# Optimization experiments

Hardware: AMD Instinct MI355X
Metric: run time of the kernel (lower is better)

## Reference

```python
import jax, jax.numpy as jnp
import numpy as np
import math

SIZE = (60, 270, 480)           # full video T, H, W
CHANNELS = 14                   # sum of per-level grid channels 8+4+2
GRID_SIZES = [(60, 16, 16, 8), (30, 8, 8, 4), (15, 4, 4, 2)]
IDX_MAX = (60, 3, 5)            # patch grid -> patch_size (1, 90, 96)
PADDING = (0, 1, 1)
N_PATCH = 64
MANIP_LBASE = 2.0
MANIP_LEVELS = 8
INIT_SCALE = 1e-3


def setup_inputs() -> dict:
    key = jax.random.key(0)
    kt, kh, kw = jax.random.split(key, 3)
    idx = jnp.stack([
        jax.random.randint(kt, (N_PATCH,), 0, IDX_MAX[0]),
        jax.random.randint(kh, (N_PATCH,), 0, IDX_MAX[1]),
        jax.random.randint(kw, (N_PATCH,), 0, IDX_MAX[2]),
    ], axis=1).astype(jnp.int32)
    inp = {
        "idx": idx,
        "idx_max": jnp.asarray(IDX_MAX, dtype=jnp.int32),
        "padding": jnp.asarray(PADDING, dtype=jnp.int32),
    }
    for i, (T, H, W, C) in enumerate(GRID_SIZES):
        k = jax.random.fold_in(key, 10 + i)
        inp[f"grid{i}"] = jax.random.normal(k, (T * H * W, C), jnp.float32) * INIT_SCALE
    return inp


def _pixel_idx_1d(ix, size_d, nmax_d, pad_d):
    # ix: [N] patch index along one dim -> ([N, P+2*pad] clipped pixel idx, mask)
    p = size_d // nmax_d
    offs = jnp.arange(-pad_d, p + pad_d)
    raw = ix[:, None] * p + offs[None, :]
    mask = ((raw >= 0) & (raw < size_d)).astype(jnp.float32)
    return jnp.clip(raw, 0, size_d - 1), mask


def reference(idx, idx_max, padding, grid0, grid1, grid2):
    T, H, W = SIZE
    im = tuple(int(v) for v in np.asarray(idx_max))
    pad = tuple(int(v) for v in np.asarray(padding))
    patch = tuple(SIZE[d] // im[d] for d in range(3))
    ppad = tuple(patch[d] + 2 * pad[d] for d in range(3))

    # Multi-level grids -> trilinear upsample to full (T,H,W,C_i), concat on C.
    # jax.image.resize 'trilinear' uses half-pixel centers == torch align_corners=False.
    enc_splits = []
    for g, (Tg, Hg, Wg, Cg) in zip((grid0, grid1, grid2), GRID_SIZES):
        enc_splits.append(jax.image.resize(g.reshape(Tg, Hg, Wg, Cg), (T, H, W, Cg), method="trilinear"))
    enc = jnp.concatenate(enc_splits, axis=-1).reshape(T * H * W, CHANNELS)

    it, mt = _pixel_idx_1d(idx[:, 0], T, im[0], pad[0])
    ih, mh = _pixel_idx_1d(idx[:, 1], H, im[1], pad[1])
    iw, mw = _pixel_idx_1d(idx[:, 2], W, im[2], pad[2])

    flat = (it[:, :, None, None] * (H * W) + ih[:, None, :, None] * W + iw[:, None, None, :]).reshape(-1)
    mask = (mt[:, :, None, None] * mh[:, None, :, None] * mw[:, None, None, :]).reshape(-1, 1)

    t_embed = (mask * enc[flat]).reshape((idx.shape[0],) + ppad + (CHANNELS,))

    bases = (MANIP_LBASE ** jnp.arange(MANIP_LEVELS, dtype=jnp.float32)) * math.pi
    v = idx[:, 0].astype(jnp.float32)[:, None] * bases
    t_manip = jnp.concatenate([jnp.sin(v), jnp.cos(v)], axis=-1)  # [N, 2*levels]

    return t_embed, t_manip
```

## Files before the change

### kernel.cpp

```cpp
#include <hip/hip_runtime.h>
#include <math.h>


#define N_PATCH 64
#define PPAD_H 92
#define PPAD_W 98
#define CH 14
#define PIX_PER_PATCH (PPAD_H * PPAD_W)
#define ROWS_PER_BLOCK 2
#define BLOCKS_PER_PATCH 46
#define PX_PER_BLOCK 196
#define F4_PER_BLOCK (PX_PER_BLOCK * CH / 4)
#define ELEMS_PER_PATCH (PIX_PER_PATCH * CH)
#define ELEMS_PER_BLOCK (PX_PER_BLOCK * CH)
#define TOTAL_EMBED (N_PATCH * ELEMS_PER_PATCH)
#define TOTAL_MANIP (N_PATCH * 16)

#define RB_STRIDE 72
#define L1_OFF 48
#define L2_OFF 64

__device__ __forceinline__ float lerpf(float a, float b, float f) {
    return a + f * (b - a);
}

__device__ __forceinline__ int wcell0(int rw0, float sw, int Wg) {
    float x = ((float)rw0 + 0.5f) * sw - 0.5f;
    int w0 = (int)floorf(x);
    return min(max(w0, 0), Wg - 1);
}

__global__ __launch_bounds__(256) void embed_kernel(
    const int* __restrict__ idx,
    const float* __restrict__ g0,
    const float* __restrict__ g1,
    const float* __restrict__ g2,
    float* __restrict__ out)
{
    __shared__ __align__(16) float s_V[ROWS_PER_BLOCK * RB_STRIDE];
    __shared__ __align__(16) float s_buf[PX_PER_BLOCK * CH];

    const int tid = threadIdx.x;
    const int bx  = blockIdx.x;
    const int n   = blockIdx.y;
    const int it  = idx[3 * n + 0];
    const int ih  = idx[3 * n + 1];
    const int iw  = idx[3 * n + 2];
    const int rw0 = iw * 96 - 1;

    const float sw0 = (float)((double)16 / 480.0);
    const float sw1 = (float)((double)8  / 480.0);
    const float sw2 = (float)((double)4  / 480.0);
    const float sh0 = (float)((double)16 / 270.0);
    const float sh1 = (float)((double)8  / 270.0);
    const float sh2 = (float)((double)4  / 270.0);

    const int C0_0 = wcell0(rw0, sw0, 16);
    const int C0_1 = wcell0(rw0, sw1, 8);
    const int C0_2 = wcell0(rw0, sw2, 4);

    if (bx == 0 && n == 0) {
        float* om = out + TOTAL_EMBED;
        for (int e = tid; e < TOTAL_MANIP; e += 256) {
            int nn = e >> 4;
            int j  = e & 15;
            int l  = j & 7;
            float base = (float)M_PI * (float)(1 << l);
            float v = (float)idx[3 * nn + 0] * base;
            double dv = (double)v;
            om[e] = (float)((j < 8) ? sin(dv) : cos(dv));
        }
    }

    if (tid < 96) {
        int chn  = tid & 7;
        int u    = tid >> 3;
        int row  = (u >= 6);
        int cell = u - 6 * row;
        int rh   = ih * 90 + (bx * 2 + row) - 1;
        float mh = ((unsigned)rh < 270u) ? 1.0f : 0.0f;
        float xh = ((float)rh + 0.5f) * sh0 - 0.5f;
        float ff = floorf(xh);
        float fh = xh - ff;
        int h0 = (int)ff;
        int h0c = min(max(h0, 0), 15), h1c = min(h0 + 1, 15);
        int cw = min(C0_0 + cell, 15);
        const float* base = g0 + (size_t)it * 2048;
        float a = base[(h0c * 16 + cw) * 8 + chn];
        float b = base[(h1c * 16 + cw) * 8 + chn];
        s_V[row * RB_STRIDE + cell * 8 + chn] = mh * lerpf(a, b, fh);
    } else if (tid < 128) {
        int i    = tid - 96;
        int chn  = i & 3;
        int u    = i >> 2;
        int row  = (u >= 4);
        int cell = u - 4 * row;
        int rh   = ih * 90 + (bx * 2 + row) - 1;
        float mh = ((unsigned)rh < 270u) ? 1.0f : 0.0f;
        float xh = ((float)rh + 0.5f) * sh1 - 0.5f;
        float ff = floorf(xh);
        float fh = xh - ff;
        int h0 = (int)ff;
        int h0c = min(max(h0, 0), 7), h1c = min(h0 + 1, 7);
        float xt = ((float)it + 0.5f) * 0.5f - 0.5f;
        float ftf = floorf(xt);
        float ft  = xt - ftf;
        int t0 = (int)ftf;
        int t0c = min(max(t0, 0), 29), t1c = min(t0 + 1, 29);
        int cw = min(C0_1 + cell, 7);
        float a00 = g1[((t0c * 8 + h0c) * 8 + cw) * 4 + chn];
        float a01 = g1[((t0c * 8 + h1c) * 8 + cw) * 4 + chn];
        float a10 = g1[((t1c * 8 + h0c) * 8 + cw) * 4 + chn];
        float a11 = g1[((t1c * 8 + h1c) * 8 + cw) * 4 + chn];
        s_V[row * RB_STRIDE + L1_OFF + cell * 4 + chn] =
            mh * lerpf(lerpf(a00, a01, fh), lerpf(a10, a11, fh), ft);
    } else if (tid < 140) {
        int i    = tid - 128;
        int chn  = i & 1;
        int u    = i >> 1;
        int row  = (u >= 3);
        int cell = u - 3 * row;
        int rh   = ih * 90 + (bx * 2 + row) - 1;
        float mh = ((unsigned)rh < 270u) ? 1.0f : 0.0f;
        float xh = ((float)rh + 0.5f) * sh2 - 0.5f;
        float ff = floorf(xh);
        float fh = xh - ff;
        int h0 = (int)ff;
        int h0c = min(max(h0, 0), 3), h1c = min(h0 + 1, 3);
        float xt = ((float)it + 0.5f) * 0.25f - 0.5f;
        float ftf = floorf(xt);
        float ft  = xt - ftf;
        int t0 = (int)ftf;
        int t0c = min(max(t0, 0), 14), t1c = min(t0 + 1, 14);
        int cw = min(C0_2 + cell, 3);
        float a00 = g2[((t0c * 4 + h0c) * 4 + cw) * 2 + chn];
        float a01 = g2[((t0c * 4 + h1c) * 4 + cw) * 2 + chn];
        float a10 = g2[((t1c * 4 + h0c) * 4 + cw) * 2 + chn];
        float a11 = g2[((t1c * 4 + h1c) * 4 + cw) * 2 + chn];
        s_V[row * RB_STRIDE + L2_OFF + cell * 2 + chn] =
            mh * lerpf(lerpf(a00, a01, fh), lerpf(a10, a11, fh), ft);
    }

    __syncthreads();

    if (tid < PX_PER_BLOCK) {
        int row = (tid >= PPAD_W);
        int ww  = tid - PPAD_W * row;
        int rw  = iw * 96 + ww - 1;
        float mw = ((unsigned)rw < 480u) ? 1.0f : 0.0f;
        float rwc = (float)rw + 0.5f;

        float x0 = rwc * sw0 - 0.5f;
        float f0f = floorf(x0);
        float fw0 = x0 - f0f;
        int w00 = (int)f0f;
        int oA0 = (min(max(w00, 0), 15) - C0_0) * 8;
        int oB0 = (min(w00 + 1, 15)    - C0_0) * 8;
        float x1 = rwc * sw1 - 0.5f;
        float f1f = floorf(x1);
        float fw1 = x1 - f1f;
        int w01 = (int)f1f;
        int oA1 = L1_OFF + (min(max(w01, 0), 7) - C0_1) * 4;
        int oB1 = L1_OFF + (min(w01 + 1, 7)     - C0_1) * 4;
        float x2 = rwc * sw2 - 0.5f;
        float f2f = floorf(x2);
        float fw2 = x2 - f2f;
        int w02 = (int)f2f;
        int oA2 = L2_OFF + (min(max(w02, 0), 3) - C0_2) * 2;
        int oB2 = L2_OFF + (min(w02 + 1, 3)     - C0_2) * 2;

        const float* V = s_V + row * RB_STRIDE;
        float4 A0  = *(const float4*)(V + oA0);
        float4 A1  = *(const float4*)(V + oA0 + 4);
        float4 B0  = *(const float4*)(V + oB0);
        float4 B1  = *(const float4*)(V + oB0 + 4);
        float4 C1a = *(const float4*)(V + oA1);
        float4 C1b = *(const float4*)(V + oB1);
        float2 C2a = *(const float2*)(V + oA2);
        float2 C2b = *(const float2*)(V + oB2);

        float2* b = (float2*)(s_buf + tid * CH);
        b[0] = make_float2(mw * lerpf(A0.x, B0.x, fw0),
                           mw * lerpf(A0.y, B0.y, fw0));
        b[1] = make_float2(mw * lerpf(A0.z, B0.z, fw0),
                           mw * lerpf(A0.w, B0.w, fw0));
        b[2] = make_float2(mw * lerpf(A1.x, B1.x, fw0),
                           mw * lerpf(A1.y, B1.y, fw0));
        b[3] = make_float2(mw * lerpf(A1.z, B1.z, fw0),
                           mw * lerpf(A1.w, B1.w, fw0));
        b[4] = make_float2(mw * lerpf(C1a.x, C1b.x, fw1),
                           mw * lerpf(C1a.y, C1b.y, fw1));
        b[5] = make_float2(mw * lerpf(C1a.z, C1b.z, fw1),
                           mw * lerpf(C1a.w, C1b.w, fw1));
        b[6] = make_float2(mw * lerpf(C2a.x, C2b.x, fw2),
                           mw * lerpf(C2a.y, C2b.y, fw2));
    }
    __syncthreads();

    const float4* sb = (const float4*)s_buf;
    float4* gb = (float4*)(out + (size_t)n * ELEMS_PER_PATCH + bx * ELEMS_PER_BLOCK);
    for (int j = tid; j < F4_PER_BLOCK; j += 256) gb[j] = sb[j];
}

extern "C" void kernel_launch(void* const* d_in, const int* in_sizes, int n_in,
                              void* d_out, int out_size, void* d_ws, size_t ws_size,
                              hipStream_t stream) {
    const int*   idx = (const int*)  d_in[0];
    const float* g0  = (const float*)d_in[3];
    const float* g1  = (const float*)d_in[4];
    const float* g2  = (const float*)d_in[5];
    float* out = (float*)d_out;

    dim3 grid(BLOCKS_PER_PATCH, N_PATCH);
    embed_kernel<<<grid, 256, 0, stream>>>(idx, g0, g1, g2, out);
}
```

Before: 12.64 us.

## Process two patches per block, overlapping one tile's store with next compute

Each block now handles two patches (n and n+32), halving the grid. The row-interpolation stage for both patches is done in one loop, then the first tile is computed, stored while the second tile is computed, and the second tile is stored. This aims to amortize per-block setup and overlap global stores with compute, at the cost of fewer blocks (1472 vs 2944), double shared memory, and more serialized work per block.

Result: slower. 14.07 us (+11.3%).

```diff
diff --git a/kernel.cpp b/kernel.cpp
--- a/kernel.cpp
+++ b/kernel.cpp
@@ -3,6 +3,7 @@
 
 
 #define N_PATCH 64
+#define HALF_N 32
 #define PPAD_H 92
 #define PPAD_W 98
 #define CH 14
@@ -37,16 +38,15 @@
     const float* __restrict__ g2,
     float* __restrict__ out)
 {
-    __shared__ __align__(16) float s_V[ROWS_PER_BLOCK * RB_STRIDE];
-    __shared__ __align__(16) float s_buf[PX_PER_BLOCK * CH];
+    __shared__ __align__(16) float s_V0[ROWS_PER_BLOCK * RB_STRIDE];
+    __shared__ __align__(16) float s_V1[ROWS_PER_BLOCK * RB_STRIDE];
+    __shared__ __align__(16) float s_buf0[PX_PER_BLOCK * CH];
+    __shared__ __align__(16) float s_buf1[PX_PER_BLOCK * CH];
 
     const int tid = threadIdx.x;
     const int bx  = blockIdx.x;
-    const int n   = blockIdx.y;
-    const int it  = idx[3 * n + 0];
-    const int ih  = idx[3 * n + 1];
-    const int iw  = idx[3 * n + 2];
-    const int rw0 = iw * 96 - 1;
+    const int n0  = blockIdx.y;
+    const int n1  = blockIdx.y + HALF_N;
 
     const float sw0 = (float)((double)16 / 480.0);
     const float sw1 = (float)((double)8  / 480.0);
@@ -55,11 +55,14 @@
     const float sh1 = (float)((double)8  / 270.0);
     const float sh2 = (float)((double)4  / 270.0);
 
-    const int C0_0 = wcell0(rw0, sw0, 16);
-    const int C0_1 = wcell0(rw0, sw1, 8);
-    const int C0_2 = wcell0(rw0, sw2, 4);
-
-    if (bx == 0 && n == 0) {
+    const int it0 = idx[3 * n0 + 0], ih0 = idx[3 * n0 + 1], iw0 = idx[3 * n0 + 2];
+    const int it1 = idx[3 * n1 + 0], ih1 = idx[3 * n1 + 1], iw1 = idx[3 * n1 + 2];
+    const int rw0a = iw0 * 96 - 1;
+    const int rw0b = iw1 * 96 - 1;
+    const int C00a = wcell0(rw0a, sw0, 16), C01a = wcell0(rw0a, sw1, 8), C02a = wcell0(rw0a, sw2, 4);
+    const int C00b = wcell0(rw0b, sw0, 16), C01b = wcell0(rw0b, sw1, 8), C02b = wcell0(rw0b, sw2, 4);
+
+    if (bx == 0 && blockIdx.y == 0) {
         float* om = out + TOTAL_EMBED;
         for (int e = tid; e < TOTAL_MANIP; e += 256) {
             int nn = e >> 4;
@@ -72,81 +75,80 @@
         }
     }
 
-    if (tid < 96) {
-        int chn  = tid & 7;
-        int u    = tid >> 3;
-        int row  = (u >= 6);
-        int cell = u - 6 * row;
-        int rh   = ih * 90 + (bx * 2 + row) - 1;
+    for (int e = tid; e < 280; e += 256) {
+        int t   = (e >= 140);
+        int oa  = e - 140 * t;
+        int row = (oa >= 70);
+        int off = oa - 70 * row;
+        int itq = t ? it1 : it0;
+        int ihq = t ? ih1 : ih0;
+        float* sV = t ? s_V1 : s_V0;
+        int rh  = ihq * 90 + (bx * 2 + row) - 1;
         float mh = ((unsigned)rh < 270u) ? 1.0f : 0.0f;
-        float xh = ((float)rh + 0.5f) * sh0 - 0.5f;
-        float ff = floorf(xh);
-        float fh = xh - ff;
-        int h0 = (int)ff;
-        int h0c = min(max(h0, 0), 15), h1c = min(h0 + 1, 15);
-        int cw = min(C0_0 + cell, 15);
-        const float* base = g0 + (size_t)it * 2048;
-        float a = base[(h0c * 16 + cw) * 8 + chn];
-        float b = base[(h1c * 16 + cw) * 8 + chn];
-        s_V[row * RB_STRIDE + cell * 8 + chn] = mh * lerpf(a, b, fh);
-    } else if (tid < 128) {
-        int i    = tid - 96;
-        int chn  = i & 3;
-        int u    = i >> 2;
-        int row  = (u >= 4);
-        int cell = u - 4 * row;
-        int rh   = ih * 90 + (bx * 2 + row) - 1;
-        float mh = ((unsigned)rh < 270u) ? 1.0f : 0.0f;
-        float xh = ((float)rh + 0.5f) * sh1 - 0.5f;
-        float ff = floorf(xh);
-        float fh = xh - ff;
-        int h0 = (int)ff;
-        int h0c = min(max(h0, 0), 7), h1c = min(h0 + 1, 7);
-        float xt = ((float)it + 0.5f) * 0.5f - 0.5f;
-        float ftf = floorf(xt);
-        float ft  = xt - ftf;
-        int t0 = (int)ftf;
-        int t0c = min(max(t0, 0), 29), t1c = min(t0 + 1, 29);
-        int cw = min(C0_1 + cell, 7);
-        float a00 = g1[((t0c * 8 + h0c) * 8 + cw) * 4 + chn];
-        float a01 = g1[((t0c * 8 + h1c) * 8 + cw) * 4 + chn];
-        float a10 = g1[((t1c * 8 + h0c) * 8 + cw) * 4 + chn];
-        float a11 = g1[((t1c * 8 + h1c) * 8 + cw) * 4 + chn];
-        s_V[row * RB_STRIDE + L1_OFF + cell * 4 + chn] =
-            mh * lerpf(lerpf(a00, a01, fh), lerpf(a10, a11, fh), ft);
-    } else if (tid < 140) {
-        int i    = tid - 128;
-        int chn  = i & 1;
-        int u    = i >> 1;
-        int row  = (u >= 3);
-        int cell = u - 3 * row;
-        int rh   = ih * 90 + (bx * 2 + row) - 1;
-        float mh = ((unsigned)rh < 270u) ? 1.0f : 0.0f;
-        float xh = ((float)rh + 0.5f) * sh2 - 0.5f;
-        float ff = floorf(xh);
-        float fh = xh - ff;
-        int h0 = (int)ff;
-        int h0c = min(max(h0, 0), 3), h1c = min(h0 + 1, 3);
-        float xt = ((float)it + 0.5f) * 0.25f - 0.5f;
-        float ftf = floorf(xt);
-        float ft  = xt - ftf;
-        int t0 = (int)ftf;
-        int t0c = min(max(t0, 0), 14), t1c = min(t0 + 1, 14);
-        int cw = min(C0_2 + cell, 3);
-        float a00 = g2[((t0c * 4 + h0c) * 4 + cw) * 2 + chn];
-        float a01 = g2[((t0c * 4 + h1c) * 4 + cw) * 2 + chn];
-        float a10 = g2[((t1c * 4 + h0c) * 4 + cw) * 2 + chn];
-        float a11 = g2[((t1c * 4 + h1c) * 4 + cw) * 2 + chn];
-        s_V[row * RB_STRIDE + L2_OFF + cell * 2 + chn] =
-            mh * lerpf(lerpf(a00, a01, fh), lerpf(a10, a11, fh), ft);
+        float v;
+        if (off < L1_OFF) {
+            int C00q = t ? C00b : C00a;
+            int cell = off >> 3, chn = off & 7;
+            float xh = ((float)rh + 0.5f) * sh0 - 0.5f;
+            float ff = floorf(xh);
+            float fh = xh - ff;
+            int h0 = (int)ff;
+            int h0c = min(max(h0, 0), 15), h1c = min(h0 + 1, 15);
+            int cw = min(C00q + cell, 15);
+            const float* base = g0 + (size_t)itq * 2048;
+            float a = base[(h0c * 16 + cw) * 8 + chn];
+            float b = base[(h1c * 16 + cw) * 8 + chn];
+            v = mh * lerpf(a, b, fh);
+        } else if (off < L2_OFF) {
+            int C01q = t ? C01b : C01a;
+            int o = off - L1_OFF;
+            int cell = o >> 2, chn = o & 3;
+            float xh = ((float)rh + 0.5f) * sh1 - 0.5f;
+            float ff = floorf(xh);
+            float fh = xh - ff;
+            int h0 = (int)ff;
+            int h0c = min(max(h0, 0), 7), h1c = min(h0 + 1, 7);
+            float xt = ((float)itq + 0.5f) * 0.5f - 0.5f;
+            float ftf = floorf(xt);
+            float ft  = xt - ftf;
+            int t0 = (int)ftf;
+            int t0c = min(max(t0, 0), 29), t1c = min(t0 + 1, 29);
+            int cw = min(C01q + cell, 7);
+            float a00 = g1[((t0c * 8 + h0c) * 8 + cw) * 4 + chn];
+            float a01 = g1[((t0c * 8 + h1c) * 8 + cw) * 4 + chn];
+            float a10 = g1[((t1c * 8 + h0c) * 8 + cw) * 4 + chn];
+            float a11 = g1[((t1c * 8 + h1c) * 8 + cw) * 4 + chn];
+            v = mh * lerpf(lerpf(a00, a01, fh), lerpf(a10, a11, fh), ft);
+        } else {
+            int C02q = t ? C02b : C02a;
+            int o = off - L2_OFF;
+            int cell = o >> 1, chn = o & 1;
+            float xh = ((float)rh + 0.5f) * sh2 - 0.5f;
+            float ff = floorf(xh);
+            float fh = xh - ff;
+            int h0 = (int)ff;
+            int h0c = min(max(h0, 0), 3), h1c = min(h0 + 1, 3);
+            float xt = ((float)itq + 0.5f) * 0.25f - 0.5f;
+            float ftf = floorf(xt);
+            float ft  = xt - ftf;
+            int t0 = (int)ftf;
+            int t0c = min(max(t0, 0), 14), t1c = min(t0 + 1, 14);
+            int cw = min(C02q + cell, 3);
+            float a00 = g2[((t0c * 4 + h0c) * 4 + cw) * 2 + chn];
+            float a01 = g2[((t0c * 4 + h1c) * 4 + cw) * 2 + chn];
+            float a10 = g2[((t1c * 4 + h0c) * 4 + cw) * 2 + chn];
+            float a11 = g2[((t1c * 4 + h1c) * 4 + cw) * 2 + chn];
+            v = mh * lerpf(lerpf(a00, a01, fh), lerpf(a10, a11, fh), ft);
+        }
+        sV[row * RB_STRIDE + off] = v;
     }
 
-    __syncthreads();
-
-    if (tid < PX_PER_BLOCK) {
+    auto compute_tile = [&](int iwq, int C00q, int C01q, int C02q,
+                            const float* __restrict__ sV, float* __restrict__ sbuf) {
+        if (tid >= PX_PER_BLOCK) return;
         int row = (tid >= PPAD_W);
         int ww  = tid - PPAD_W * row;
-        int rw  = iw * 96 + ww - 1;
+        int rw  = iwq * 96 + ww - 1;
         float mw = ((unsigned)rw < 480u) ? 1.0f : 0.0f;
         float rwc = (float)rw + 0.5f;
 
@@ -154,22 +156,22 @@
         float f0f = floorf(x0);
         float fw0 = x0 - f0f;
         int w00 = (int)f0f;
-        int oA0 = (min(max(w00, 0), 15) - C0_0) * 8;
-        int oB0 = (min(w00 + 1, 15)    - C0_0) * 8;
+        int oA0 = (min(max(w00, 0), 15) - C00q) * 8;
+        int oB0 = (min(w00 + 1, 15)    - C00q) * 8;
         float x1 = rwc * sw1 - 0.5f;
         float f1f = floorf(x1);
         float fw1 = x1 - f1f;
         int w01 = (int)f1f;
-        int oA1 = L1_OFF + (min(max(w01, 0), 7) - C0_1) * 4;
-        int oB1 = L1_OFF + (min(w01 + 1, 7)     - C0_1) * 4;
+        int oA1 = L1_OFF + (min(max(w01, 0), 7) - C01q) * 4;
+        int oB1 = L1_OFF + (min(w01 + 1, 7)     - C01q) * 4;
         float x2 = rwc * sw2 - 0.5f;
         float f2f = floorf(x2);
         float fw2 = x2 - f2f;
         int w02 = (int)f2f;
-        int oA2 = L2_OFF + (min(max(w02, 0), 3) - C0_2) * 2;
-        int oB2 = L2_OFF + (min(w02 + 1, 3)     - C0_2) * 2;
-
-        const float* V = s_V + row * RB_STRIDE;
+        int oA2 = L2_OFF + (min(max(w02, 0), 3) - C02q) * 2;
+        int oB2 = L2_OFF + (min(w02 + 1, 3)     - C02q) * 2;
+
+        const float* V = sV + row * RB_STRIDE;
         float4 A0  = *(const float4*)(V + oA0);
         float4 A1  = *(const float4*)(V + oA0 + 4);
         float4 B0  = *(const float4*)(V + oB0);
@@ -179,7 +181,7 @@
         float2 C2a = *(const float2*)(V + oA2);
         float2 C2b = *(const float2*)(V + oB2);
 
-        float2* b = (float2*)(s_buf + tid * CH);
+        float2* b = (float2*)(sbuf + tid * CH);
         b[0] = make_float2(mw * lerpf(A0.x, B0.x, fw0),
                            mw * lerpf(A0.y, B0.y, fw0));
         b[1] = make_float2(mw * lerpf(A0.z, B0.z, fw0),
@@ -194,12 +196,24 @@
                            mw * lerpf(C1a.w, C1b.w, fw1));
         b[6] = make_float2(mw * lerpf(C2a.x, C2b.x, fw2),
                            mw * lerpf(C2a.y, C2b.y, fw2));
-    }
+    };
+
+    auto store_tile = [&](int nq, const float* __restrict__ sbuf) {
+        const float4* sb = (const float4*)sbuf;
+        float4* gb = (float4*)(out + (size_t)nq * ELEMS_PER_PATCH + bx * ELEMS_PER_BLOCK);
+        for (int j = tid; j < F4_PER_BLOCK; j += 256) gb[j] = sb[j];
+    };
+
     __syncthreads();
 
-    const float4* sb = (const float4*)s_buf;
-    float4* gb = (float4*)(out + (size_t)n * ELEMS_PER_PATCH + bx * ELEMS_PER_BLOCK);
-    for (int j = tid; j < F4_PER_BLOCK; j += 256) gb[j] = sb[j];
+    compute_tile(iw0, C00a, C01a, C02a, s_V0, s_buf0);
+    __syncthreads();
+
+    store_tile(n0, s_buf0);
+    compute_tile(iw1, C00b, C01b, C02b, s_V1, s_buf1);
+    __syncthreads();
+
+    store_tile(n1, s_buf1);
 }
 
 extern "C" void kernel_launch(void* const* d_in, const int* in_sizes, int n_in,
@@ -211,6 +225,6 @@
     const float* g2  = (const float*)d_in[5];
     float* out = (float*)d_out;
 
-    dim3 grid(BLOCKS_PER_PATCH, N_PATCH);
+    dim3 grid(BLOCKS_PER_PATCH, HALF_N);
     embed_kernel<<<grid, 256, 0, stream>>>(idx, g0, g1, g2, out);
 }
```

## Split work per wavefront to replace block barriers with wave barriers

Applied to the files above, without the earlier changes.

Each of the four wavefronts now owns half a row (48 or 50 pixels) and computes its own row-interpolated grid values into a private shared slice. This replaces the block-wide __syncthreads with wave-level barriers and lgkmcnt waits, so the whole block no longer stalls while some threads load grid values. In exchange every wave redundantly fetches and interpolates the same 70 row values, and more threads (200 vs 196) do pixel work with slightly uneven store sizes per wave.

Result: slower. 13.63 us (+7.9%).

```diff
diff --git a/kernel.cpp b/kernel.cpp
--- a/kernel.cpp
+++ b/kernel.cpp
@@ -7,18 +7,21 @@
 #define PPAD_W 98
 #define CH 14
 #define PIX_PER_PATCH (PPAD_H * PPAD_W)
-#define ROWS_PER_BLOCK 2
-#define BLOCKS_PER_PATCH 46
-#define PX_PER_BLOCK 196
-#define F4_PER_BLOCK (PX_PER_BLOCK * CH / 4)
 #define ELEMS_PER_PATCH (PIX_PER_PATCH * CH)
-#define ELEMS_PER_BLOCK (PX_PER_BLOCK * CH)
+#define ELEMS_PER_BLOCK (2 * PPAD_W * CH)
 #define TOTAL_EMBED (N_PATCH * ELEMS_PER_PATCH)
 #define TOTAL_MANIP (N_PATCH * 16)
 
 #define RB_STRIDE 72
 #define L1_OFF 48
 #define L2_OFF 64
+
+#define SW0 ((float)((double)16 / 480.0))
+#define SW1 ((float)((double)8  / 480.0))
+#define SW2 ((float)((double)4  / 480.0))
+#define SH0 ((float)((double)16 / 270.0))
+#define SH1 ((float)((double)8  / 270.0))
+#define SH2 ((float)((double)4  / 270.0))
 
 __device__ __forceinline__ float lerpf(float a, float b, float f) {
     return a + f * (b - a);
@@ -37,27 +40,23 @@
     const float* __restrict__ g2,
     float* __restrict__ out)
 {
-    __shared__ __align__(16) float s_V[ROWS_PER_BLOCK * RB_STRIDE];
-    __shared__ __align__(16) float s_buf[PX_PER_BLOCK * CH];
-
-    const int tid = threadIdx.x;
-    const int bx  = blockIdx.x;
-    const int n   = blockIdx.y;
-    const int it  = idx[3 * n + 0];
-    const int ih  = idx[3 * n + 1];
-    const int iw  = idx[3 * n + 2];
+    __shared__ __align__(16) float s_V[4][RB_STRIDE];
+    __shared__ __align__(16) float s_buf[4][704];
+
+    const int tid  = threadIdx.x;
+    const int bx   = blockIdx.x;
+    const int n    = blockIdx.y;
+    const int wv   = tid >> 6;
+    const int lane = tid & 63;
+
+    const int it = idx[3 * n + 0];
+    const int ih = idx[3 * n + 1];
+    const int iw = idx[3 * n + 2];
     const int rw0 = iw * 96 - 1;
 
-    const float sw0 = (float)((double)16 / 480.0);
-    const float sw1 = (float)((double)8  / 480.0);
-    const float sw2 = (float)((double)4  / 480.0);
-    const float sh0 = (float)((double)16 / 270.0);
-    const float sh1 = (float)((double)8  / 270.0);
-    const float sh2 = (float)((double)4  / 270.0);
-
-    const int C0_0 = wcell0(rw0, sw0, 16);
-    const int C0_1 = wcell0(rw0, sw1, 8);
-    const int C0_2 = wcell0(rw0, sw2, 4);
+    const int C0_0 = wcell0(rw0, SW0, 16);
+    const int C0_1 = wcell0(rw0, SW1, 8);
+    const int C0_2 = wcell0(rw0, SW2, 4);
 
     if (bx == 0 && n == 0) {
         float* om = out + TOTAL_EMBED;
@@ -72,104 +71,101 @@
         }
     }
 
-    if (tid < 96) {
-        int chn  = tid & 7;
-        int u    = tid >> 3;
-        int row  = (u >= 6);
-        int cell = u - 6 * row;
-        int rh   = ih * 90 + (bx * 2 + row) - 1;
-        float mh = ((unsigned)rh < 270u) ? 1.0f : 0.0f;
-        float xh = ((float)rh + 0.5f) * sh0 - 0.5f;
-        float ff = floorf(xh);
-        float fh = xh - ff;
-        int h0 = (int)ff;
-        int h0c = min(max(h0, 0), 15), h1c = min(h0 + 1, 15);
-        int cw = min(C0_0 + cell, 15);
-        const float* base = g0 + (size_t)it * 2048;
-        float a = base[(h0c * 16 + cw) * 8 + chn];
-        float b = base[(h1c * 16 + cw) * 8 + chn];
-        s_V[row * RB_STRIDE + cell * 8 + chn] = mh * lerpf(a, b, fh);
-    } else if (tid < 128) {
-        int i    = tid - 96;
-        int chn  = i & 3;
-        int u    = i >> 2;
-        int row  = (u >= 4);
-        int cell = u - 4 * row;
-        int rh   = ih * 90 + (bx * 2 + row) - 1;
-        float mh = ((unsigned)rh < 270u) ? 1.0f : 0.0f;
-        float xh = ((float)rh + 0.5f) * sh1 - 0.5f;
-        float ff = floorf(xh);
-        float fh = xh - ff;
-        int h0 = (int)ff;
-        int h0c = min(max(h0, 0), 7), h1c = min(h0 + 1, 7);
-        float xt = ((float)it + 0.5f) * 0.5f - 0.5f;
-        float ftf = floorf(xt);
-        float ft  = xt - ftf;
-        int t0 = (int)ftf;
-        int t0c = min(max(t0, 0), 29), t1c = min(t0 + 1, 29);
-        int cw = min(C0_1 + cell, 7);
-        float a00 = g1[((t0c * 8 + h0c) * 8 + cw) * 4 + chn];
-        float a01 = g1[((t0c * 8 + h1c) * 8 + cw) * 4 + chn];
-        float a10 = g1[((t1c * 8 + h0c) * 8 + cw) * 4 + chn];
-        float a11 = g1[((t1c * 8 + h1c) * 8 + cw) * 4 + chn];
-        s_V[row * RB_STRIDE + L1_OFF + cell * 4 + chn] =
-            mh * lerpf(lerpf(a00, a01, fh), lerpf(a10, a11, fh), ft);
-    } else if (tid < 140) {
-        int i    = tid - 128;
-        int chn  = i & 1;
-        int u    = i >> 1;
-        int row  = (u >= 3);
-        int cell = u - 3 * row;
-        int rh   = ih * 90 + (bx * 2 + row) - 1;
-        float mh = ((unsigned)rh < 270u) ? 1.0f : 0.0f;
-        float xh = ((float)rh + 0.5f) * sh2 - 0.5f;
-        float ff = floorf(xh);
-        float fh = xh - ff;
-        int h0 = (int)ff;
-        int h0c = min(max(h0, 0), 3), h1c = min(h0 + 1, 3);
-        float xt = ((float)it + 0.5f) * 0.25f - 0.5f;
-        float ftf = floorf(xt);
-        float ft  = xt - ftf;
-        int t0 = (int)ftf;
-        int t0c = min(max(t0, 0), 14), t1c = min(t0 + 1, 14);
-        int cw = min(C0_2 + cell, 3);
-        float a00 = g2[((t0c * 4 + h0c) * 4 + cw) * 2 + chn];
-        float a01 = g2[((t0c * 4 + h1c) * 4 + cw) * 2 + chn];
-        float a10 = g2[((t1c * 4 + h0c) * 4 + cw) * 2 + chn];
-        float a11 = g2[((t1c * 4 + h1c) * 4 + cw) * 2 + chn];
-        s_V[row * RB_STRIDE + L2_OFF + cell * 2 + chn] =
-            mh * lerpf(lerpf(a00, a01, fh), lerpf(a10, a11, fh), ft);
+    const int rowloc = wv >> 1;
+    const int ww0    = (wv & 1) * 48;
+    const int npx    = 48 + 2 * (wv & 1);
+
+    const int rh = ih * 90 + bx * 2 + rowloc - 1;
+    const float mh = ((unsigned)rh < 270u) ? 1.0f : 0.0f;
+    const float rhc = (float)rh + 0.5f;
+
+    float xh0 = rhc * SH0 - 0.5f;
+    float fh0 = xh0 - floorf(xh0);
+    int   h00 = (int)floorf(xh0);
+    int   h0c0 = min(max(h00, 0), 15), h1c0 = min(h00 + 1, 15);
+
+    float xh1 = rhc * SH1 - 0.5f;
+    float fh1 = xh1 - floorf(xh1);
+    int   h01 = (int)floorf(xh1);
+    int   h0c1 = min(max(h01, 0), 7), h1c1 = min(h01 + 1, 7);
+
+    float xh2 = rhc * SH2 - 0.5f;
+    float fh2 = xh2 - floorf(xh2);
+    int   h02 = (int)floorf(xh2);
+    int   h0c2 = min(max(h02, 0), 3), h1c2 = min(h02 + 1, 3);
+
+    float xt1 = ((float)it + 0.5f) * 0.5f - 0.5f;
+    float ft1 = xt1 - floorf(xt1);
+    int   t01 = (int)floorf(xt1);
+    int   t0c1 = min(max(t01, 0), 29), t1c1 = min(t01 + 1, 29);
+
+    float xt2 = ((float)it + 0.5f) * 0.25f - 0.5f;
+    float ft2 = xt2 - floorf(xt2);
+    int   t02 = (int)floorf(xt2);
+    int   t0c2 = min(max(t02, 0), 14), t1c2 = min(t02 + 1, 14);
+
+    for (int e = lane; e < 70; e += 64) {
+        float v;
+        if (e < L1_OFF) {
+            int cell = e >> 3, chn = e & 7;
+            int cw = min(C0_0 + cell, 15);
+            const float* b0 = g0 + (size_t)it * 2048;
+            float a = b0[(h0c0 * 16 + cw) * 8 + chn];
+            float b = b0[(h1c0 * 16 + cw) * 8 + chn];
+            v = mh * lerpf(a, b, fh0);
+        } else if (e < L2_OFF) {
+            int o = e - L1_OFF;
+            int cell = o >> 2, chn = o & 3;
+            int cw = min(C0_1 + cell, 7);
+            float a00 = g1[((t0c1 * 8 + h0c1) * 8 + cw) * 4 + chn];
+            float a01 = g1[((t0c1 * 8 + h1c1) * 8 + cw) * 4 + chn];
+            float a10 = g1[((t1c1 * 8 + h0c1) * 8 + cw) * 4 + chn];
+            float a11 = g1[((t1c1 * 8 + h1c1) * 8 + cw) * 4 + chn];
+            v = mh * lerpf(lerpf(a00, a01, fh1), lerpf(a10, a11, fh1), ft1);
+        } else {
+            int o = e - L2_OFF;
+            int cell = o >> 1, chn = o & 1;
+            int cw = min(C0_2 + cell, 3);
+            float a00 = g2[((t0c2 * 4 + h0c2) * 4 + cw) * 2 + chn];
+            float a01 = g2[((t0c2 * 4 + h1c2) * 4 + cw) * 2 + chn];
+            float a10 = g2[((t1c2 * 4 + h0c2) * 4 + cw) * 2 + chn];
+            float a11 = g2[((t1c2 * 4 + h1c2) * 4 + cw) * 2 + chn];
+            v = mh * lerpf(lerpf(a00, a01, fh2), lerpf(a10, a11, fh2), ft2);
+        }
+        s_V[wv][e] = v;
     }
 
-    __syncthreads();
-
-    if (tid < PX_PER_BLOCK) {
-        int row = (tid >= PPAD_W);
-        int ww  = tid - PPAD_W * row;
-        int rw  = iw * 96 + ww - 1;
+    asm volatile("s_waitcnt lgkmcnt(0)" ::: "memory");
+    __builtin_amdgcn_sched_barrier(0);
+    __builtin_amdgcn_wave_barrier();
+    __builtin_amdgcn_sched_barrier(0);
+
+    if (lane < npx) {
+        int ww = ww0 + lane;
+        int rw = iw * 96 + ww - 1;
         float mw = ((unsigned)rw < 480u) ? 1.0f : 0.0f;
         float rwc = (float)rw + 0.5f;
 
-        float x0 = rwc * sw0 - 0.5f;
+        float x0 = rwc * SW0 - 0.5f;
         float f0f = floorf(x0);
         float fw0 = x0 - f0f;
         int w00 = (int)f0f;
         int oA0 = (min(max(w00, 0), 15) - C0_0) * 8;
         int oB0 = (min(w00 + 1, 15)    - C0_0) * 8;
-        float x1 = rwc * sw1 - 0.5f;
+        float x1 = rwc * SW1 - 0.5f;
         float f1f = floorf(x1);
         float fw1 = x1 - f1f;
         int w01 = (int)f1f;
         int oA1 = L1_OFF + (min(max(w01, 0), 7) - C0_1) * 4;
         int oB1 = L1_OFF + (min(w01 + 1, 7)     - C0_1) * 4;
-        float x2 = rwc * sw2 - 0.5f;
+        float x2 = rwc * SW2 - 0.5f;
         float f2f = floorf(x2);
         float fw2 = x2 - f2f;
         int w02 = (int)f2f;
         int oA2 = L2_OFF + (min(max(w02, 0), 3) - C0_2) * 2;
         int oB2 = L2_OFF + (min(w02 + 1, 3)     - C0_2) * 2;
 
-        const float* V = s_V + row * RB_STRIDE;
+        const float* V = s_V[wv];
         float4 A0  = *(const float4*)(V + oA0);
         float4 A1  = *(const float4*)(V + oA0 + 4);
         float4 B0  = *(const float4*)(V + oB0);
@@ -179,7 +175,7 @@
         float2 C2a = *(const float2*)(V + oA2);
         float2 C2b = *(const float2*)(V + oB2);
 
-        float2* b = (float2*)(s_buf + tid * CH);
+        float2* b = (float2*)(s_buf[wv] + lane * CH);
         b[0] = make_float2(mw * lerpf(A0.x, B0.x, fw0),
                            mw * lerpf(A0.y, B0.y, fw0));
         b[1] = make_float2(mw * lerpf(A0.z, B0.z, fw0),
@@ -195,11 +191,19 @@
         b[6] = make_float2(mw * lerpf(C2a.x, C2b.x, fw2),
                            mw * lerpf(C2a.y, C2b.y, fw2));
     }
-    __syncthreads();
-
-    const float4* sb = (const float4*)s_buf;
-    float4* gb = (float4*)(out + (size_t)n * ELEMS_PER_PATCH + bx * ELEMS_PER_BLOCK);
-    for (int j = tid; j < F4_PER_BLOCK; j += 256) gb[j] = sb[j];
+
+    asm volatile("s_waitcnt lgkmcnt(0)" ::: "memory");
+    __builtin_amdgcn_sched_barrier(0);
+    __builtin_amdgcn_wave_barrier();
+    __builtin_amdgcn_sched_barrier(0);
+
+    const int p0  = rowloc * PPAD_W + ww0;
+    const int fb  = (p0 >> 1) * 7;
+    const int nf4 = (npx >> 1) * 7;
+    const float4* sb = (const float4*)s_buf[wv];
+    float4* gb = (float4*)(out + (size_t)n * ELEMS_PER_PATCH
+                               + (size_t)bx * ELEMS_PER_BLOCK) + fb;
+    for (int j = lane; j < nf4; j += 64) gb[j] = sb[j];
 }
 
 extern "C" void kernel_launch(void* const* d_in, const int* in_sizes, int n_in,
@@ -211,6 +215,6 @@
     const float* g2  = (const float*)d_in[5];
     float* out = (float*)d_out;
 
-    dim3 grid(BLOCKS_PER_PATCH, N_PATCH);
+    dim3 grid(46, N_PATCH);
     embed_kernel<<<grid, 256, 0, stream>>>(idx, g0, g1, g2, out);
 }
```

## Process two patches per block with early grid loads and LDS-only barriers

Applied to the files above, without the earlier changes.

Each block now handles two patches (n and n+32), which halves the grid. Both patches' grid gathers are issued up front into registers so their global-load latency overlaps. The barriers are replaced with LDS-only waits (lgkmcnt plus s_barrier) so that global stores from the first patch can stay in flight while the second patch is computed. This trades parallelism (fewer blocks, serialized work per block) for fewer launches and more overlap. The custom barrier also relies on s_buf reuse being safe without waiting for vmcnt.

After: 13.45 us. +6.5%, slower.

```diff
diff --git a/kernel.cpp b/kernel.cpp
--- a/kernel.cpp
+++ b/kernel.cpp
@@ -3,11 +3,11 @@
 
 
 #define N_PATCH 64
+#define HALF_N 32
 #define PPAD_H 92
 #define PPAD_W 98
 #define CH 14
 #define PIX_PER_PATCH (PPAD_H * PPAD_W)
-#define ROWS_PER_BLOCK 2
 #define BLOCKS_PER_PATCH 46
 #define PX_PER_BLOCK 196
 #define F4_PER_BLOCK (PX_PER_BLOCK * CH / 4)
@@ -20,6 +20,13 @@
 #define L1_OFF 48
 #define L2_OFF 64
 
+#define SW0 ((float)((double)16 / 480.0))
+#define SW1 ((float)((double)8  / 480.0))
+#define SW2 ((float)((double)4  / 480.0))
+#define SH0 ((float)((double)16 / 270.0))
+#define SH1 ((float)((double)8  / 270.0))
+#define SH2 ((float)((double)4  / 270.0))
+
 __device__ __forceinline__ float lerpf(float a, float b, float f) {
     return a + f * (b - a);
 }
@@ -28,6 +35,105 @@
     float x = ((float)rw0 + 0.5f) * sw - 0.5f;
     int w0 = (int)floorf(x);
     return min(max(w0, 0), Wg - 1);
+}
+
+__device__ __forceinline__ void lds_barrier() {
+    asm volatile("s_waitcnt lgkmcnt(0)" ::: "memory");
+    __builtin_amdgcn_sched_barrier(0);
+    __builtin_amdgcn_s_barrier();
+    __builtin_amdgcn_sched_barrier(0);
+}
+
+__device__ __forceinline__ float4 load_vin(int tid, int bx, int it, int ih,
+                                           int C0_0, int C0_1, int C0_2,
+                                           const float* __restrict__ g0,
+                                           const float* __restrict__ g1,
+                                           const float* __restrict__ g2)
+{
+    float4 r = make_float4(0.f, 0.f, 0.f, 0.f);
+    if (tid < 96) {
+        int chn = tid & 7, u = tid >> 3;
+        int row = (u >= 6), cell = u - 6 * row;
+        int rh = ih * 90 + (bx * 2 + row) - 1;
+        float xh = ((float)rh + 0.5f) * SH0 - 0.5f;
+        int h0 = (int)floorf(xh);
+        int h0c = min(max(h0, 0), 15), h1c = min(h0 + 1, 15);
+        int cw = min(C0_0 + cell, 15);
+        const float* base = g0 + (size_t)it * 2048;
+        r.x = base[(h0c * 16 + cw) * 8 + chn];
+        r.y = base[(h1c * 16 + cw) * 8 + chn];
+    } else if (tid < 128) {
+        int i = tid - 96;
+        int chn = i & 3, u = i >> 2;
+        int row = (u >= 4), cell = u - 4 * row;
+        int rh = ih * 90 + (bx * 2 + row) - 1;
+        float xh = ((float)rh + 0.5f) * SH1 - 0.5f;
+        int h0 = (int)floorf(xh);
+        int h0c = min(max(h0, 0), 7), h1c = min(h0 + 1, 7);
+        float xt = ((float)it + 0.5f) * 0.5f - 0.5f;
+        int t0 = (int)floorf(xt);
+        int t0c = min(max(t0, 0), 29), t1c = min(t0 + 1, 29);
+        int cw = min(C0_1 + cell, 7);
+        r.x = g1[((t0c * 8 + h0c) * 8 + cw) * 4 + chn];
+        r.y = g1[((t0c * 8 + h1c) * 8 + cw) * 4 + chn];
+        r.z = g1[((t1c * 8 + h0c) * 8 + cw) * 4 + chn];
+        r.w = g1[((t1c * 8 + h1c) * 8 + cw) * 4 + chn];
+    } else if (tid < 140) {
+        int i = tid - 128;
+        int chn = i & 1, u = i >> 1;
+        int row = (u >= 3), cell = u - 3 * row;
+        int rh = ih * 90 + (bx * 2 + row) - 1;
+        float xh = ((float)rh + 0.5f) * SH2 - 0.5f;
+        int h0 = (int)floorf(xh);
+        int h0c = min(max(h0, 0), 3), h1c = min(h0 + 1, 3);
+        float xt = ((float)it + 0.5f) * 0.25f - 0.5f;
+        int t0 = (int)floorf(xt);
+        int t0c = min(max(t0, 0), 14), t1c = min(t0 + 1, 14);
+        int cw = min(C0_2 + cell, 3);
+        r.x = g2[((t0c * 4 + h0c) * 4 + cw) * 2 + chn];
+        r.y = g2[((t0c * 4 + h1c) * 4 + cw) * 2 + chn];
+        r.z = g2[((t1c * 4 + h0c) * 4 + cw) * 2 + chn];
+        r.w = g2[((t1c * 4 + h1c) * 4 + cw) * 2 + chn];
+    }
+    return r;
+}
+
+__device__ __forceinline__ void combine_v(int tid, int bx, int it, int ih,
+                                          float4 r, float (*sV)[RB_STRIDE])
+{
+    if (tid < 96) {
+        int chn = tid & 7, u = tid >> 3;
+        int row = (u >= 6), cell = u - 6 * row;
+        int rh = ih * 90 + (bx * 2 + row) - 1;
+        float mh = ((unsigned)rh < 270u) ? 1.0f : 0.0f;
+        float xh = ((float)rh + 0.5f) * SH0 - 0.5f;
+        float fh = xh - floorf(xh);
+        sV[row][cell * 8 + chn] = mh * lerpf(r.x, r.y, fh);
+    } else if (tid < 128) {
+        int i = tid - 96;
+        int chn = i & 3, u = i >> 2;
+        int row = (u >= 4), cell = u - 4 * row;
+        int rh = ih * 90 + (bx * 2 + row) - 1;
+        float mh = ((unsigned)rh < 270u) ? 1.0f : 0.0f;
+        float xh = ((float)rh + 0.5f) * SH1 - 0.5f;
+        float fh = xh - floorf(xh);
+        float xt = ((float)it + 0.5f) * 0.5f - 0.5f;
+        float ft = xt - floorf(xt);
+        sV[row][L1_OFF + cell * 4 + chn] =
+            mh * lerpf(lerpf(r.x, r.y, fh), lerpf(r.z, r.w, fh), ft);
+    } else if (tid < 140) {
+        int i = tid - 128;
+        int chn = i & 1, u = i >> 1;
+        int row = (u >= 3), cell = u - 3 * row;
+        int rh = ih * 90 + (bx * 2 + row) - 1;
+        float mh = ((unsigned)rh < 270u) ? 1.0f : 0.0f;
+        float xh = ((float)rh + 0.5f) * SH2 - 0.5f;
+        float fh = xh - floorf(xh);
+        float xt = ((float)it + 0.5f) * 0.25f - 0.5f;
+        float ft = xt - floorf(xt);
+        sV[row][L2_OFF + cell * 2 + chn] =
+            mh * lerpf(lerpf(r.x, r.y, fh), lerpf(r.z, r.w, fh), ft);
+    }
 }
 
 __global__ __launch_bounds__(256) void embed_kernel(
@@ -37,29 +143,22 @@
     const float* __restrict__ g2,
     float* __restrict__ out)
 {
-    __shared__ __align__(16) float s_V[ROWS_PER_BLOCK * RB_STRIDE];
+    __shared__ __align__(16) float s_V0[2][RB_STRIDE];
+    __shared__ __align__(16) float s_V1[2][RB_STRIDE];
     __shared__ __align__(16) float s_buf[PX_PER_BLOCK * CH];
 
     const int tid = threadIdx.x;
     const int bx  = blockIdx.x;
-    const int n   = blockIdx.y;
-    const int it  = idx[3 * n + 0];
-    const int ih  = idx[3 * n + 1];
-    const int iw  = idx[3 * n + 2];
-    const int rw0 = iw * 96 - 1;
-
-    const float sw0 = (float)((double)16 / 480.0);
-    const float sw1 = (float)((double)8  / 480.0);
-    const float sw2 = (float)((double)4  / 480.0);
-    const float sh0 = (float)((double)16 / 270.0);
-    const float sh1 = (float)((double)8  / 270.0);
-    const float sh2 = (float)((double)4  / 270.0);
-
-    const int C0_0 = wcell0(rw0, sw0, 16);
-    const int C0_1 = wcell0(rw0, sw1, 8);
-    const int C0_2 = wcell0(rw0, sw2, 4);
-
-    if (bx == 0 && n == 0) {
+    const int n0  = blockIdx.y;
+    const int n1  = blockIdx.y + HALF_N;
+
+    const int it0 = idx[3 * n0 + 0], ih0 = idx[3 * n0 + 1], iw0 = idx[3 * n0 + 2];
+    const int it1 = idx[3 * n1 + 0], ih1 = idx[3 * n1 + 1], iw1 = idx[3 * n1 + 2];
+    const int rw0a = iw0 * 96 - 1, rw0b = iw1 * 96 - 1;
+    const int C00a = wcell0(rw0a, SW0, 16), C01a = wcell0(rw0a, SW1, 8), C02a = wcell0(rw0a, SW2, 4);
+    const int C00b = wcell0(rw0b, SW0, 16), C01b = wcell0(rw0b, SW1, 8), C02b = wcell0(rw0b, SW2, 4);
+
+    if (bx == 0 && blockIdx.y == 0) {
         float* om = out + TOTAL_EMBED;
         for (int e = tid; e < TOTAL_MANIP; e += 256) {
             int nn = e >> 4;
@@ -72,104 +171,38 @@
         }
     }
 
-    if (tid < 96) {
-        int chn  = tid & 7;
-        int u    = tid >> 3;
-        int row  = (u >= 6);
-        int cell = u - 6 * row;
-        int rh   = ih * 90 + (bx * 2 + row) - 1;
-        float mh = ((unsigned)rh < 270u) ? 1.0f : 0.0f;
-        float xh = ((float)rh + 0.5f) * sh0 - 0.5f;
-        float ff = floorf(xh);
-        float fh = xh - ff;
-        int h0 = (int)ff;
-        int h0c = min(max(h0, 0), 15), h1c = min(h0 + 1, 15);
-        int cw = min(C0_0 + cell, 15);
-        const float* base = g0 + (size_t)it * 2048;
-        float a = base[(h0c * 16 + cw) * 8 + chn];
-        float b = base[(h1c * 16 + cw) * 8 + chn];
-        s_V[row * RB_STRIDE + cell * 8 + chn] = mh * lerpf(a, b, fh);
-    } else if (tid < 128) {
-        int i    = tid - 96;
-        int chn  = i & 3;
-        int u    = i >> 2;
-        int row  = (u >= 4);
-        int cell = u - 4 * row;
-        int rh   = ih * 90 + (bx * 2 + row) - 1;
-        float mh = ((unsigned)rh < 270u) ? 1.0f : 0.0f;
-        float xh = ((float)rh + 0.5f) * sh1 - 0.5f;
-        float ff = floorf(xh);
-        float fh = xh - ff;
-        int h0 = (int)ff;
-        int h0c = min(max(h0, 0), 7), h1c = min(h0 + 1, 7);
-        float xt = ((float)it + 0.5f) * 0.5f - 0.5f;
-        float ftf = floorf(xt);
-        float ft  = xt - ftf;
-        int t0 = (int)ftf;
-        int t0c = min(max(t0, 0), 29), t1c = min(t0 + 1, 29);
-        int cw = min(C0_1 + cell, 7);
-        float a00 = g1[((t0c * 8 + h0c) * 8 + cw) * 4 + chn];
-        float a01 = g1[((t0c * 8 + h1c) * 8 + cw) * 4 + chn];
-        float a10 = g1[((t1c * 8 + h0c) * 8 + cw) * 4 + chn];
-        float a11 = g1[((t1c * 8 + h1c) * 8 + cw) * 4 + chn];
-        s_V[row * RB_STRIDE + L1_OFF + cell * 4 + chn] =
-            mh * lerpf(lerpf(a00, a01, fh), lerpf(a10, a11, fh), ft);
-    } else if (tid < 140) {
-        int i    = tid - 128;
-        int chn  = i & 1;
-        int u    = i >> 1;
-        int row  = (u >= 3);
-        int cell = u - 3 * row;
-        int rh   = ih * 90 + (bx * 2 + row) - 1;
-        float mh = ((unsigned)rh < 270u) ? 1.0f : 0.0f;
-        float xh = ((float)rh + 0.5f) * sh2 - 0.5f;
-        float ff = floorf(xh);
-        float fh = xh - ff;
-        int h0 = (int)ff;
-        int h0c = min(max(h0, 0), 3), h1c = min(h0 + 1, 3);
-        float xt = ((float)it + 0.5f) * 0.25f - 0.5f;
-        float ftf = floorf(xt);
-        float ft  = xt - ftf;
-        int t0 = (int)ftf;
-        int t0c = min(max(t0, 0), 14), t1c = min(t0 + 1, 14);
-        int cw = min(C0_2 + cell, 3);
-        float a00 = g2[((t0c * 4 + h0c) * 4 + cw) * 2 + chn];
-        float a01 = g2[((t0c * 4 + h1c) * 4 + cw) * 2 + chn];
-        float a10 = g2[((t1c * 4 + h0c) * 4 + cw) * 2 + chn];
-        float a11 = g2[((t1c * 4 + h1c) * 4 + cw) * 2 + chn];
-        s_V[row * RB_STRIDE + L2_OFF + cell * 2 + chn] =
-            mh * lerpf(lerpf(a00, a01, fh), lerpf(a10, a11, fh), ft);
-    }
-
-    __syncthreads();
-
-    if (tid < PX_PER_BLOCK) {
+    float4 r0 = load_vin(tid, bx, it0, ih0, C00a, C01a, C02a, g0, g1, g2);
+    float4 r1 = load_vin(tid, bx, it1, ih1, C00b, C01b, C02b, g0, g1, g2);
+
+    auto compute_tile = [&](int iwq, int C00q, int C01q, int C02q,
+                            const float (*sV)[RB_STRIDE]) {
+        if (tid >= PX_PER_BLOCK) return;
         int row = (tid >= PPAD_W);
         int ww  = tid - PPAD_W * row;
-        int rw  = iw * 96 + ww - 1;
+        int rw  = iwq * 96 + ww - 1;
         float mw = ((unsigned)rw < 480u) ? 1.0f : 0.0f;
         float rwc = (float)rw + 0.5f;
 
-        float x0 = rwc * sw0 - 0.5f;
+        float x0 = rwc * SW0 - 0.5f;
         float f0f = floorf(x0);
         float fw0 = x0 - f0f;
         int w00 = (int)f0f;
-        int oA0 = (min(max(w00, 0), 15) - C0_0) * 8;
-        int oB0 = (min(w00 + 1, 15)    - C0_0) * 8;
-        float x1 = rwc * sw1 - 0.5f;
+        int oA0 = (min(max(w00, 0), 15) - C00q) * 8;
+        int oB0 = (min(w00 + 1, 15)    - C00q) * 8;
+        float x1 = rwc * SW1 - 0.5f;
         float f1f = floorf(x1);
         float fw1 = x1 - f1f;
         int w01 = (int)f1f;
-        int oA1 = L1_OFF + (min(max(w01, 0), 7) - C0_1) * 4;
-        int oB1 = L1_OFF + (min(w01 + 1, 7)     - C0_1) * 4;
-        float x2 = rwc * sw2 - 0.5f;
+        int oA1 = L1_OFF + (min(max(w01, 0), 7) - C01q) * 4;
+        int oB1 = L1_OFF + (min(w01 + 1, 7)     - C01q) * 4;
+        float x2 = rwc * SW2 - 0.5f;
         float f2f = floorf(x2);
         float fw2 = x2 - f2f;
         int w02 = (int)f2f;
-        int oA2 = L2_OFF + (min(max(w02, 0), 3) - C0_2) * 2;
-        int oB2 = L2_OFF + (min(w02 + 1, 3)     - C0_2) * 2;
-
-        const float* V = s_V + row * RB_STRIDE;
+        int oA2 = L2_OFF + (min(max(w02, 0), 3) - C02q) * 2;
+        int oB2 = L2_OFF + (min(w02 + 1, 3)     - C02q) * 2;
+
+        const float* V = sV[row];
         float4 A0  = *(const float4*)(V + oA0);
         float4 A1  = *(const float4*)(V + oA0 + 4);
         float4 B0  = *(const float4*)(V + oB0);
@@ -194,12 +227,28 @@
                            mw * lerpf(C1a.w, C1b.w, fw1));
         b[6] = make_float2(mw * lerpf(C2a.x, C2b.x, fw2),
                            mw * lerpf(C2a.y, C2b.y, fw2));
-    }
-    __syncthreads();
-
-    const float4* sb = (const float4*)s_buf;
-    float4* gb = (float4*)(out + (size_t)n * ELEMS_PER_PATCH + bx * ELEMS_PER_BLOCK);
-    for (int j = tid; j < F4_PER_BLOCK; j += 256) gb[j] = sb[j];
+    };
+
+    auto store_tile = [&](int nq) {
+        const float4* sb = (const float4*)s_buf;
+        float4* gb = (float4*)(out + (size_t)nq * ELEMS_PER_PATCH + bx * ELEMS_PER_BLOCK);
+        for (int j = tid; j < F4_PER_BLOCK; j += 256) gb[j] = sb[j];
+    };
+
+    combine_v(tid, bx, it0, ih0, r0, s_V0);
+    lds_barrier();
+
+    compute_tile(iw0, C00a, C01a, C02a, s_V0);
+    lds_barrier();
+
+    store_tile(n0);
+    combine_v(tid, bx, it1, ih1, r1, s_V1);
+    lds_barrier();
+
+    compute_tile(iw1, C00b, C01b, C02b, s_V1);
+    lds_barrier();
+
+    store_tile(n1);
 }
 
 extern "C" void kernel_launch(void* const* d_in, const int* in_sizes, int n_in,
@@ -211,6 +260,6 @@
     const float* g2  = (const float*)d_in[5];
     float* out = (float*)d_out;
 
-    dim3 grid(BLOCKS_PER_PATCH, N_PATCH);
+    dim3 grid(BLOCKS_PER_PATCH, HALF_N);
     embed_kernel<<<grid, 256, 0, stream>>>(idx, g0, g1, g2, out);
 }
```
